# Kernel tuning notes

Hardware: AMD Instinct MI355X
Metric: run time of the kernel (lower is better)

Reference implementation:

```python
import jax, jax.numpy as jnp
import numpy as np

NUM_HEADS = 16
D_MODEL = 1024
D_K = D_MODEL // NUM_HEADS


def setup_inputs() -> dict:
    key = jax.random.key(0)
    ks = jax.random.split(key, 6)
    B, S = 4, 2048
    x = jax.random.normal(ks[0], (B, S, D_MODEL), dtype=jnp.float32)
    scale = 1.0 / np.sqrt(D_MODEL)
    W_q = jax.random.normal(ks[1], (D_MODEL, D_MODEL), dtype=jnp.float32) * scale
    W_k = jax.random.normal(ks[2], (D_MODEL, D_MODEL), dtype=jnp.float32) * scale
    W_v = jax.random.normal(ks[3], (D_MODEL, D_MODEL), dtype=jnp.float32) * scale
    W_o = jax.random.normal(ks[4], (D_MODEL, D_MODEL), dtype=jnp.float32) * scale
    b_o = jnp.zeros((D_MODEL,), dtype=jnp.float32)
    return {"x": x, "W_q": W_q, "W_k": W_k, "W_v": W_v, "W_o": W_o, "b_o": b_o}


def reference(x, W_q, W_k, W_v, W_o, b_o):
    B, S, D = x.shape
    H, dk = NUM_HEADS, D_K
    # torch nn.Linear computes x @ W.T
    q = (x @ W_q.T).reshape(B, S, H, dk).transpose(0, 2, 1, 3)  # [B,H,S,dk]
    k = (x @ W_k.T).reshape(B, S, H, dk).transpose(0, 2, 1, 3)
    v = (x @ W_v.T).reshape(B, S, H, dk).transpose(0, 2, 1, 3)
    scores = jnp.einsum('bhqd,bhkd->bhqk', q, k) / jnp.sqrt(jnp.float32(dk))
    causal = jnp.tril(jnp.ones((S, S), dtype=bool))  # allowed positions
    scores = jnp.where(causal[None, None], scores, -jnp.inf)
    attn = jax.nn.softmax(scores, axis=-1)
    out = jnp.einsum('bhqk,bhkd->bhqd', attn, v)
    combined = out.transpose(0, 2, 1, 3).reshape(B, S, D)
    return combined @ W_o.T + b_o
```

## Files before the change

### kernel.cpp

```cpp
#include <hip/hip_runtime.h>

typedef __attribute__((ext_vector_type(8))) short short8;
typedef __attribute__((ext_vector_type(4))) float f32x4;

#define GLOAD16(gp, lp)                                                        \
  __builtin_amdgcn_global_load_lds(                                            \
      (const __attribute__((address_space(1))) void*)(gp),                     \
      (__attribute__((address_space(3))) void*)(lp), 16, 0, 0)

__device__ __forceinline__ unsigned short f2bf(float f) {
  unsigned int u = __builtin_bit_cast(unsigned int, f);
  u += 0x7fffu + ((u >> 16) & 1u);
  return (unsigned short)(u >> 16);
}

__global__ __launch_bounds__(256) void cvt_f32_bf16(
    const float* __restrict__ src, unsigned short* __restrict__ dst, int n,
    float scale) {
  int i = (blockIdx.x * 256 + threadIdx.x) * 8;
  if (i + 8 <= n) {
    float4 a = *(const float4*)(src + i);
    float4 b = *(const float4*)(src + i + 4);
    short8 r;
    r[0] = (short)f2bf(a.x * scale); r[1] = (short)f2bf(a.y * scale);
    r[2] = (short)f2bf(a.z * scale); r[3] = (short)f2bf(a.w * scale);
    r[4] = (short)f2bf(b.x * scale); r[5] = (short)f2bf(b.y * scale);
    r[6] = (short)f2bf(b.z * scale); r[7] = (short)f2bf(b.w * scale);
    *(short8*)(dst + i) = r;
  }
}

__global__ __launch_bounds__(256) void cvt_w4(
    const float* __restrict__ Wq, const float* __restrict__ Wk,
    const float* __restrict__ Wv, const float* __restrict__ Wo,
    unsigned short* __restrict__ Wqkv, unsigned short* __restrict__ Wob,
    int DD, float qscale) {
  const int y = blockIdx.y;
  const float* src = (y == 0) ? Wq : (y == 1) ? Wk : (y == 2) ? Wv : Wo;
  unsigned short* dst = (y < 3) ? Wqkv + (size_t)y * DD : Wob;
  const float scale = (y == 0) ? qscale : 1.0f;
  int i = (blockIdx.x * 256 + threadIdx.x) * 8;
  if (i + 8 <= DD) {
    float4 a = *(const float4*)(src + i);
    float4 b = *(const float4*)(src + i + 4);
    short8 r;
    r[0] = (short)f2bf(a.x * scale); r[1] = (short)f2bf(a.y * scale);
    r[2] = (short)f2bf(a.z * scale); r[3] = (short)f2bf(a.w * scale);
    r[4] = (short)f2bf(b.x * scale); r[5] = (short)f2bf(b.y * scale);
    r[6] = (short)f2bf(b.z * scale); r[7] = (short)f2bf(b.w * scale);
    *(short8*)(dst + i) = r;
  }
}

template <int BN, int OUTF32>
__global__ __launch_bounds__(512) void gemm_nt2(
    const unsigned short* __restrict__ A, const unsigned short* __restrict__ B,
    void* __restrict__ Cout, const float* __restrict__ bias, int M, int N,
    int K, int nwg_y) {
  constexpr int NF = BN / 64;
  constexpr int WNSZ = BN / 4;
  __shared__ __align__(16) unsigned short As[2][256][64];
  __shared__ __align__(16) unsigned short Bs[2][BN][64];

  const int nwg = gridDim.x;
  const int id = blockIdx.x;
  const int sw = (id & 7) * (nwg >> 3) + (id >> 3);
  const int bx = sw / nwg_y, by = sw % nwg_y;
  const int row0 = bx * 256, col0 = by * BN;

  const int tid = threadIdx.x;
  const int wave = tid >> 6, lane = tid & 63;
  const int wm = wave >> 2, wn = wave & 3;
  const int l15 = lane & 15, l16 = lane >> 4;
  const int lrow = lane >> 3, lcol = (lane & 7) * 8;
  const int wv8 = wave * 8;

  f32x4 acc[8][NF];
#pragma unroll
  for (int m = 0; m < 8; ++m)
#pragma unroll
    for (int n = 0; n < NF; ++n) acc[m][n] = f32x4{0.f, 0.f, 0.f, 0.f};

  const int nt = K >> 6;

#define STAGE_TILE(buf, k0)                                                    \
  {                                                                            \
    _Pragma("unroll") for (int j = 0; j < 4; ++j) {                            \
      const unsigned short* gp =                                               \
          A + (size_t)(row0 + j * 64 + wv8 + lrow) * K + (k0) + lcol;          \
      GLOAD16(gp, &As[buf][j * 64 + wv8][0]);                                  \
    }                                                                          \
    _Pragma("unroll") for (int j = 0; j < NF; ++j) {                           \
      const unsigned short* gp =                                               \
          B + (size_t)(col0 + j * 64 + wv8 + lrow) * K + (k0) + lcol;          \
      GLOAD16(gp, &Bs[buf][j * 64 + wv8][0]);                                  \
    }                                                                          \
  }

  STAGE_TILE(0, 0)
  __syncthreads();

  for (int t = 0; t < nt; ++t) {
    const int cur = t & 1;
    if (t + 1 < nt) STAGE_TILE(cur ^ 1, (t + 1) << 6)

#pragma unroll
    for (int kk = 0; kk < 2; ++kk) {
      short8 a[8], b[NF];
#pragma unroll
      for (int m = 0; m < 8; ++m)
        a[m] = *(const short8*)&As[cur][wm * 128 + m * 16 + l15][kk * 32 + l16 * 8];
#pragma unroll
      for (int n = 0; n < NF; ++n)
        b[n] = *(const short8*)&Bs[cur][wn * WNSZ + n * 16 + l15][kk * 32 + l16 * 8];
#pragma unroll
      for (int m = 0; m < 8; ++m)
#pragma unroll
        for (int n = 0; n < NF; ++n)
          acc[m][n] =
              __builtin_amdgcn_mfma_f32_16x16x32_bf16(a[m], b[n], acc[m][n], 0, 0, 0);
    }
    __syncthreads();
  }

#pragma unroll
  for (int m = 0; m < 8; ++m) {
    const int row = row0 + wm * 128 + m * 16 + l16 * 4;
#pragma unroll
    for (int n = 0; n < NF; ++n) {
      const int col = col0 + wn * WNSZ + n * 16 + l15;
      float bv = 0.f;
      if (OUTF32) bv = bias[col];
#pragma unroll
      for (int r = 0; r < 4; ++r) {
        const float v = acc[m][n][r] + bv;
        if (OUTF32)
          ((float*)Cout)[(size_t)(row + r) * N + col] = v;
        else
          ((unsigned short*)Cout)[(size_t)(row + r) * N + col] = f2bf(v);
      }
    }
  }
#undef STAGE_TILE
}

__device__ __forceinline__ int kvperm(int slot) {
  const int s = slot >> 4, l = (slot >> 2) & 3, rr = slot & 3;
  return 32 * (s & 1) + 8 * l + 4 * (s >> 1) + rr;
}

__global__ __launch_bounds__(512) void attn_fwd(
    const unsigned short* __restrict__ QKV, unsigned short* __restrict__ AO) {
  const int S = 2048, LD = 3072;
  const int qt = gridDim.x - 1 - blockIdx.x;
  const int bh = blockIdx.y, b = bh >> 4, h = bh & 15;
  const int tid = threadIdx.x, wave = tid >> 6, lane = tid & 63;
  const int l15 = lane & 15, l16 = lane >> 4;
  const int q0 = qt * 128;

  __shared__ __align__(16) char KsB[2][64 * 128];
  __shared__ __align__(16) char VTB[2][64 * 128];

  const unsigned short* qptr =
      QKV + (size_t)(b * S + q0 + wave * 16 + l15) * LD + h * 64 + l16 * 8;
  short8 qf[2];
  qf[0] = *(const short8*)(qptr);
  qf[1] = *(const short8*)(qptr + 32);

  const int krow = lane >> 3;
  const int kcol = (((lane & 7) ^ (lane >> 3)) & 7) * 8;
  int kvp[2];
#pragma unroll
  for (int i = 0; i < 2; ++i)
    kvp[i] = kvperm(((wave - 4) * 2 + i) * 8 + krow);
  const int vp_ = tid & 31, vd0 = ((tid >> 5) & 7) * 8;

  float mrow = -1e30f, lsum = 0.f;
  f32x4 accO[4] = {};
  const int nkv = 2 * qt + 2;
  const int koff8 = 8 * l16;

  {
    if (wave >= 4) {
#pragma unroll
      for (int i = 0; i < 2; ++i) {
        const int c = (wave - 4) * 2 + i;
        const unsigned short* gp =
            QKV + (size_t)(b * S + kvp[i]) * LD + 1024 + h * 64 + kcol;
        GLOAD16(gp, KsB[0] + c * 1024);
      }
    } else {
      const unsigned short* vp =
          QKV + (size_t)(b * S + 2 * vp_) * LD + 2048 + h * 64 + vd0;
      short8 va = *(const short8*)vp;
      short8 vb = *(const short8*)(vp + LD);
      uint4 vaw = __builtin_bit_cast(uint4, va);
      uint4 vbw = __builtin_bit_cast(uint4, vb);
      const unsigned int aw[4] = {vaw.x, vaw.y, vaw.z, vaw.w};
      const unsigned int bw[4] = {vbw.x, vbw.y, vbw.z, vbw.w};
#pragma unroll
      for (int w = 0; w < 4; ++w) {
        unsigned int e = __builtin_amdgcn_perm(bw[w], aw[w], 0x05040100u);
        unsigned int o = __builtin_amdgcn_perm(bw[w], aw[w], 0x07060302u);
        *(unsigned int*)(VTB[0] + (((vd0 + 2 * w) * 128 + 4 * vp_) ^ ((2 * w) << 4))) = e;
        *(unsigned int*)(VTB[0] + (((vd0 + 2 * w + 1) * 128 + 4 * vp_) ^ ((2 * w + 1) << 4))) = o;
      }
    }
  }
  __syncthreads();

  for (int t = 0; t < nkv; ++t) {
    const int cur = t & 1, kv0 = t * 64;

    f32x4 accS[4] = {};
#pragma unroll
    for (int sub = 0; sub < 4; ++sub) {
      const int rw = sub * 16 + l15;
#pragma unroll
      for (int kk = 0; kk < 2; ++kk) {
        short8 kf = *(const short8*)(KsB[cur] + rw * 128 +
                                     ((kk * 64 + l16 * 16) ^ ((l15 & 7) << 4)));
        accS[sub] =
            __builtin_amdgcn_mfma_f32_16x16x32_bf16(kf, qf[kk], accS[sub], 0, 0, 0);
      }
    }

    short8 va, vb;
    const bool pre = (t + 1 < nkv);
    if (pre) {
      const int kvn = kv0 + 64;
      if (wave >= 4) {
#pragma unroll
        for (int i = 0; i < 2; ++i) {
          const int c = (wave - 4) * 2 + i;
          const unsigned short* gp =
              QKV + (size_t)(b * S + kvn + kvp[i]) * LD + 1024 + h * 64 + kcol;
          GLOAD16(gp, KsB[cur ^ 1] + c * 1024);
        }
      } else {
        const unsigned short* vp =
            QKV + (size_t)(b * S + kvn + 2 * vp_) * LD + 2048 + h * 64 + vd0;
        va = *(const short8*)vp;
        vb = *(const short8*)(vp + LD);
      }
    }

    const bool nm = (kv0 + 63 > q0 + wave * 16);
    float mx = -1e30f;
    if (nm) {
      const int qabs = q0 + wave * 16 + l15;
#pragma unroll
      for (int sub = 0; sub < 4; ++sub) {
        const int kbase = kv0 + 32 * (sub & 1) + 4 * (sub >> 1) + koff8;
#pragma unroll
        for (int r = 0; r < 4; ++r) {
          float s = accS[sub][r];
          if (kbase + r > qabs) s = -1e30f;
          accS[sub][r] = s;
          mx = fmaxf(mx, s);
        }
      }
    } else {
#pragma unroll
      for (int sub = 0; sub < 4; ++sub)
#pragma unroll
        for (int r = 0; r < 4; ++r) mx = fmaxf(mx, accS[sub][r]);
    }
    mx = fmaxf(mx, __shfl_xor(mx, 16));
    mx = fmaxf(mx, __shfl_xor(mx, 32));

    if (__any(mx > mrow + 8.0f)) {
      const float mnew = fmaxf(mrow, mx);
      const float alpha = exp2f(mrow - mnew);
      mrow = mnew;
      lsum *= alpha;
#pragma unroll
      for (int sd = 0; sd < 4; ++sd)
#pragma unroll
        for (int r = 0; r < 4; ++r) accO[sd][r] *= alpha;
    }

    float rs = 0.f;
#pragma unroll
    for (int sub = 0; sub < 4; ++sub)
#pragma unroll
      for (int r = 0; r < 4; ++r) {
        const float pv = exp2f(accS[sub][r] - mrow);
        accS[sub][r] = pv;
        rs += pv;
      }
    rs += __shfl_xor(rs, 16);
    rs += __shfl_xor(rs, 32);
    lsum += rs;

    short8 pf[2];
#pragma unroll
    for (int kk = 0; kk < 2; ++kk) {
      unsigned int w0, w1, w2, w3;
      asm("v_cvt_pk_bf16_f32 %0, %1, %2" : "=v"(w0) : "v"(accS[kk][0]), "v"(accS[kk][1]));
      asm("v_cvt_pk_bf16_f32 %0, %1, %2" : "=v"(w1) : "v"(accS[kk][2]), "v"(accS[kk][3]));
      asm("v_cvt_pk_bf16_f32 %0, %1, %2" : "=v"(w2) : "v"(accS[kk + 2][0]), "v"(accS[kk + 2][1]));
      asm("v_cvt_pk_bf16_f32 %0, %1, %2" : "=v"(w3) : "v"(accS[kk + 2][2]), "v"(accS[kk + 2][3]));
      uint4 u = {w0, w1, w2, w3};
      pf[kk] = __builtin_bit_cast(short8, u);
    }

    if (pre && wave < 4) {
      uint4 vaw = __builtin_bit_cast(uint4, va);
      uint4 vbw = __builtin_bit_cast(uint4, vb);
      const unsigned int aw[4] = {vaw.x, vaw.y, vaw.z, vaw.w};
      const unsigned int bw[4] = {vbw.x, vbw.y, vbw.z, vbw.w};
#pragma unroll
      for (int w = 0; w < 4; ++w) {
        unsigned int e = __builtin_amdgcn_perm(bw[w], aw[w], 0x05040100u);
        unsigned int o = __builtin_amdgcn_perm(bw[w], aw[w], 0x07060302u);
        *(unsigned int*)(VTB[cur ^ 1] +
                         (((vd0 + 2 * w) * 128 + 4 * vp_) ^ ((2 * w) << 4))) = e;
        *(unsigned int*)(VTB[cur ^ 1] +
                         (((vd0 + 2 * w + 1) * 128 + 4 * vp_) ^ ((2 * w + 1) << 4))) = o;
      }
    }

#pragma unroll
    for (int kk = 0; kk < 2; ++kk) {
#pragma unroll
      for (int sd = 0; sd < 4; ++sd) {
        short8 vf = *(const short8*)(VTB[cur] + (sd * 16 + l15) * 128 +
                                     ((kk * 64 + l16 * 16) ^ ((l15 & 7) << 4)));
        accO[sd] =
            __builtin_amdgcn_mfma_f32_16x16x32_bf16(vf, pf[kk], accO[sd], 0, 0, 0);
      }
    }
    __syncthreads();
  }

  const float inv = __builtin_amdgcn_rcpf(lsum);
  unsigned short* aop =
      AO + (size_t)(b * S + q0 + wave * 16 + l15) * 1024 + h * 64;
#pragma unroll
  for (int sd = 0; sd < 4; ++sd) {
    const int d = sd * 16 + l16 * 4;
    unsigned int w0, w1;
    float o0 = accO[sd][0] * inv, o1 = accO[sd][1] * inv;
    float o2 = accO[sd][2] * inv, o3 = accO[sd][3] * inv;
    asm("v_cvt_pk_bf16_f32 %0, %1, %2" : "=v"(w0) : "v"(o0), "v"(o1));
    asm("v_cvt_pk_bf16_f32 %0, %1, %2" : "=v"(w1) : "v"(o2), "v"(o3));
    *(unsigned int*)(aop + d) = w0;
    *(unsigned int*)(aop + d + 2) = w1;
  }
}

extern "C" void kernel_launch(void* const* d_in, const int* in_sizes, int n_in,
                              void* d_out, int out_size, void* d_ws,
                              size_t ws_size, hipStream_t stream) {
  const float* x = (const float*)d_in[0];
  const float* Wq = (const float*)d_in[1];
  const float* Wk = (const float*)d_in[2];
  const float* Wv = (const float*)d_in[3];
  const float* Wo = (const float*)d_in[4];
  const float* bo = (const float*)d_in[5];

  char* ws = (char*)d_ws;
  unsigned short* xb = (unsigned short*)(ws);
  unsigned short* Wqkv = (unsigned short*)(ws + (size_t)(16 << 20));
  unsigned short* Wob = (unsigned short*)(ws + (size_t)(22 << 20));
  unsigned short* QKV = (unsigned short*)(ws + (size_t)(24 << 20));
  unsigned short* AO = (unsigned short*)(ws + (size_t)(72 << 20));

  const int M = 8192, D = 1024;
  const float QSCALE = 0.125f * 1.44269504088896340736f;

  cvt_f32_bf16<<<M * D / 2048, 256, 0, stream>>>(x, xb, M * D, 1.0f);
  dim3 gw(D * D / 2048, 4);
  cvt_w4<<<gw, 256, 0, stream>>>(Wq, Wk, Wv, Wo, Wqkv, Wob, D * D, QSCALE);

  gemm_nt2<192, 0><<<(M / 256) * (3072 / 192), 512, 0, stream>>>(
      xb, Wqkv, QKV, nullptr, M, 3072, D, 3072 / 192);

  dim3 g2(16, 64);
  attn_fwd<<<g2, 512, 0, stream>>>(QKV, AO);

  gemm_nt2<128, 1><<<(M / 256) * (D / 128), 512, 0, stream>>>(
      AO, Wob, d_out, bo, M, D, D, D / 128);
}
```

Measured before the change: 322.3 us.

## Triple-buffer GEMM LDS with XOR swizzle, fine-grained vmcnt waits, and setprio

Replaces the double-buffered GEMM with a triple-buffered version that prefetches two K-tiles ahead and waits on vmcnt counts instead of a full __syncthreads. LDS rows are XOR-swizzled to cut bank conflicts on the MFMA operand reads. MFMA sections are raised with s_setprio. The QKV projection tile drops from BN=192 to 128, which launches more workgroups with fewer accumulators each; the larger LDS footprint (144KB) may limit occupancy.

```diff
diff --git a/kernel.cpp b/kernel.cpp
--- a/kernel.cpp
+++ b/kernel.cpp
@@ -52,83 +52,97 @@
   }
 }
 
-template <int BN, int OUTF32>
-__global__ __launch_bounds__(512) void gemm_nt2(
+template <int OUTF32>
+__global__ __launch_bounds__(512) void gemm_nt3(
     const unsigned short* __restrict__ A, const unsigned short* __restrict__ B,
     void* __restrict__ Cout, const float* __restrict__ bias, int M, int N,
     int K, int nwg_y) {
-  constexpr int NF = BN / 64;
-  constexpr int WNSZ = BN / 4;
-  __shared__ __align__(16) unsigned short As[2][256][64];
-  __shared__ __align__(16) unsigned short Bs[2][BN][64];
+  __shared__ __align__(16) unsigned short As[3][256][64];
+  __shared__ __align__(16) unsigned short Bs[3][128][64];
 
   const int nwg = gridDim.x;
   const int id = blockIdx.x;
   const int sw = (id & 7) * (nwg >> 3) + (id >> 3);
   const int bx = sw / nwg_y, by = sw % nwg_y;
-  const int row0 = bx * 256, col0 = by * BN;
+  const int row0 = bx * 256, col0 = by * 128;
 
   const int tid = threadIdx.x;
   const int wave = tid >> 6, lane = tid & 63;
   const int wm = wave >> 2, wn = wave & 3;
   const int l15 = lane & 15, l16 = lane >> 4;
-  const int lrow = lane >> 3, lcol = (lane & 7) * 8;
-  const int wv8 = wave * 8;
-
-  f32x4 acc[8][NF];
+  const int srow = lane >> 3;
+  const int scol = ((lane & 7) ^ srow) * 8;
+
+  f32x4 acc[8][2];
 #pragma unroll
   for (int m = 0; m < 8; ++m)
 #pragma unroll
-    for (int n = 0; n < NF; ++n) acc[m][n] = f32x4{0.f, 0.f, 0.f, 0.f};
+    for (int n = 0; n < 2; ++n) acc[m][n] = f32x4{0.f, 0.f, 0.f, 0.f};
 
   const int nt = K >> 6;
 
-#define STAGE_TILE(buf, k0)                                                    \
+#define STAGE3(buf, k0)                                                        \
   {                                                                            \
     _Pragma("unroll") for (int j = 0; j < 4; ++j) {                            \
-      const unsigned short* gp =                                               \
-          A + (size_t)(row0 + j * 64 + wv8 + lrow) * K + (k0) + lcol;          \
-      GLOAD16(gp, &As[buf][j * 64 + wv8][0]);                                  \
+      const int c = wave * 4 + j;                                              \
+      GLOAD16(A + (size_t)(row0 + c * 8 + srow) * K + (k0) + scol,             \
+              &As[buf][c * 8][0]);                                             \
     }                                                                          \
-    _Pragma("unroll") for (int j = 0; j < NF; ++j) {                           \
-      const unsigned short* gp =                                               \
-          B + (size_t)(col0 + j * 64 + wv8 + lrow) * K + (k0) + lcol;          \
-      GLOAD16(gp, &Bs[buf][j * 64 + wv8][0]);                                  \
+    _Pragma("unroll") for (int j = 0; j < 2; ++j) {                            \
+      const int c = wave * 2 + j;                                              \
+      GLOAD16(B + (size_t)(col0 + c * 8 + srow) * K + (k0) + scol,             \
+              &Bs[buf][c * 8][0]);                                             \
     }                                                                          \
   }
 
-  STAGE_TILE(0, 0)
-  __syncthreads();
+  STAGE3(0, 0)
+  STAGE3(1, 64)
 
   for (int t = 0; t < nt; ++t) {
-    const int cur = t & 1;
-    if (t + 1 < nt) STAGE_TILE(cur ^ 1, (t + 1) << 6)
-
+    const int cur = t % 3;
+    if (t + 2 < nt) STAGE3((t + 2) % 3, (t + 2) << 6)
+
+    if (t + 2 < nt) {
+      asm volatile("s_waitcnt vmcnt(12)" ::: "memory");
+    } else if (t + 1 < nt) {
+      asm volatile("s_waitcnt vmcnt(6)" ::: "memory");
+    } else {
+      asm volatile("s_waitcnt vmcnt(0)" ::: "memory");
+    }
+    __builtin_amdgcn_sched_barrier(0);
+    __builtin_amdgcn_s_barrier();
+
+    const char* Ab = (const char*)&As[cur][0][0];
+    const char* Bb = (const char*)&Bs[cur][0][0];
+    __builtin_amdgcn_s_setprio(1);
 #pragma unroll
     for (int kk = 0; kk < 2; ++kk) {
-      short8 a[8], b[NF];
+      const int co = (kk * 64 + l16 * 16) ^ ((l15 & 7) << 4);
+      short8 a[8], b[2];
 #pragma unroll
       for (int m = 0; m < 8; ++m)
-        a[m] = *(const short8*)&As[cur][wm * 128 + m * 16 + l15][kk * 32 + l16 * 8];
-#pragma unroll
-      for (int n = 0; n < NF; ++n)
-        b[n] = *(const short8*)&Bs[cur][wn * WNSZ + n * 16 + l15][kk * 32 + l16 * 8];
+        a[m] = *(const short8*)(Ab + (wm * 128 + m * 16 + l15) * 128 + co);
+#pragma unroll
+      for (int n = 0; n < 2; ++n)
+        b[n] = *(const short8*)(Bb + (wn * 32 + n * 16 + l15) * 128 + co);
 #pragma unroll
       for (int m = 0; m < 8; ++m)
 #pragma unroll
-        for (int n = 0; n < NF; ++n)
+        for (int n = 0; n < 2; ++n)
           acc[m][n] =
               __builtin_amdgcn_mfma_f32_16x16x32_bf16(a[m], b[n], acc[m][n], 0, 0, 0);
     }
-    __syncthreads();
-  }
+    __builtin_amdgcn_s_setprio(0);
+    __builtin_amdgcn_s_barrier();
+  }
+#undef STAGE3
 
 #pragma unroll
   for (int m = 0; m < 8; ++m) {
     const int row = row0 + wm * 128 + m * 16 + l16 * 4;
 #pragma unroll
-    for (int n = 0; n < NF; ++n) {
-      const int col = col0 + wn * WNSZ + n * 16 + l15;
+    for (int n = 0; n < 2; ++n) {
+      const int col = col0 + wn * 32 + n * 16 + l15;
       float bv = 0.f;
       if (OUTF32) bv = bias[col];
 #pragma unroll
@@ -141,7 +155,6 @@
       }
     }
   }
-#undef STAGE_TILE
 }
 
 __device__ __forceinline__ int kvperm(int slot) {
@@ -374,12 +387,12 @@
   dim3 gw(D * D / 2048, 4);
   cvt_w4<<<gw, 256, 0, stream>>>(Wq, Wk, Wv, Wo, Wqkv, Wob, D * D, QSCALE);
 
-  gemm_nt2<192, 0><<<(M / 256) * (3072 / 192), 512, 0, stream>>>(
-      xb, Wqkv, QKV, nullptr, M, 3072, D, 3072 / 192);
+  gemm_nt3<0><<<(M / 256) * (3072 / 128), 512, 0, stream>>>(
+      xb, Wqkv, QKV, nullptr, M, 3072, D, 3072 / 128);
 
   dim3 g2(16, 64);
   attn_fwd<<<g2, 512, 0, stream>>>(QKV, AO);
 
-  gemm_nt2<128, 1><<<(M / 256) * (D / 128), 512, 0, stream>>>(
+  gemm_nt3<1><<<(M / 256) * (D / 128), 512, 0, stream>>>(
       AO, Wob, d_out, bo, M, D, D, D / 128);
 }
```

Measured after the change: 313.8 us. 2.6% less time.
